# Optimization experiments

Hardware: AMD Instinct MI355X
Metric: run time of the kernel (lower is better)

Reference implementation:

```python
import jax, jax.numpy as jnp
import numpy as np
import math

D = 1024
H = 16
HD = D // H


def setup_inputs() -> dict:
    key = jax.random.key(0)
    ks = jax.random.split(key, 12)
    B, L = 2, 2048
    s = 1.0 / math.sqrt(D)
    inp = {
        "q": jax.random.normal(ks[0], (B, L, D), jnp.float32),
        "k": jax.random.normal(ks[1], (B, L, D), jnp.float32),
        "v": jax.random.normal(ks[2], (B, L, D), jnp.float32),
        "Wq": jax.random.normal(ks[3], (D, D), jnp.float32) * s,
        "bq": jnp.zeros((D,), jnp.float32),
        "Wk": jax.random.normal(ks[4], (D, D), jnp.float32) * s,
        "bk": jnp.zeros((D,), jnp.float32),
        "Wv": jax.random.normal(ks[5], (D, D), jnp.float32) * s,
        "bv": jnp.zeros((D,), jnp.float32),
        "Wo": jax.random.normal(ks[6], (D, D), jnp.float32) * s,
        "bo": jnp.zeros((D,), jnp.float32),
        "P": jax.random.normal(ks[7], (H, H), jnp.float32),  # logit_proj_pre
    }
    return inp


def _split_heads(x, B, L):
    # [B,L,D] -> [B,H,L,HD]
    return x.reshape(B, L, H, HD).transpose(0, 2, 1, 3)


def reference(q, k, v, Wq, bq, Wk, bk, Wv, bv, Wo, bo, P):
    B, L, _ = q.shape
    qh = _split_heads(q @ Wq.T + bq, B, L)
    kh = _split_heads(k @ Wk.T + bk, B, L)
    vh = _split_heads(v @ Wv.T + bv, B, L)
    # raw per-head logits [B,H,L,L]
    logits = jnp.einsum("bhld,bhmd->bhlm", qh, kh) / math.sqrt(HD)
    # talking-heads mixing across heads (pre-softmax)
    logits = jnp.einsum("bhlm,hg->bglm", logits, P)
    attn = jax.nn.softmax(logits, axis=-1)
    out = jnp.einsum("bhlm,bhmd->bhld", attn, vh)  # [B,H,L,HD]
    out = out.transpose(0, 2, 1, 3).reshape(B, L, D)
    return out @ Wo.T + bo
```

## Files before the change

### kernel.cpp

```cpp
#include <hip/hip_runtime.h>

#define D_  1024
#define H_  16
#define HD_ 64
#define L_  2048
#define B_  2
#define M_  (B_*L_)

typedef float f32x4  __attribute__((ext_vector_type(4)));
typedef short bf16x4 __attribute__((ext_vector_type(4)));
typedef short bf16x8 __attribute__((ext_vector_type(8)));

__device__ __forceinline__ float bf2f(short s) {
    return __uint_as_float(((unsigned int)(unsigned short)s) << 16);
}
__device__ __forceinline__ short f2bf(float f) {
    unsigned u = __float_as_uint(f);
    unsigned r = (u + 0x7FFFu + ((u >> 16) & 1u)) >> 16;
    return (short)r;
}

__global__ __launch_bounds__(256) void proj_mfma(
    const float* __restrict__ q, const float* __restrict__ k, const float* __restrict__ v,
    const float* __restrict__ Wq, const float* __restrict__ bq,
    const float* __restrict__ Wk, const float* __restrict__ bk,
    const float* __restrict__ Wv, const float* __restrict__ bv,
    short* __restrict__ qh, short* __restrict__ qlo,
    short* __restrict__ kh, short* __restrict__ vht)
{
    const int z = blockIdx.z;
    const float* X    = (z == 0) ? q  : (z == 1) ? k  : v;
    const float* W    = (z == 0) ? Wq : (z == 1) ? Wk : Wv;
    const float* bias = (z == 0) ? bq : (z == 1) ? bk : bv;

    __shared__ short Ws[128][40];
    __shared__ short Xs[128][40];

    const int tid  = threadIdx.x;
    const int w    = tid >> 6, lane = tid & 63;
    const int l16  = lane & 15, qq = lane >> 4;
    const int m0   = blockIdx.x * 128;
    const int n0   = blockIdx.y * 128;
    const int ar0  = 64 * (w & 1);
    const int br0  = 64 * (w >> 1);

    f32x4 acc[4][4] = {};

    for (int k0 = 0; k0 < D_; k0 += 32) {
        #pragma unroll
        for (int i = 0; i < 4; ++i) {
            int fidx = i * 256 + tid;
            int r = fidx >> 3, c = fidx & 7;
            float4 wv4 = *(const float4*)(W + (size_t)(n0 + r) * D_ + k0 + c * 4);
            float4 xv4 = *(const float4*)(X + (size_t)(m0 + r) * D_ + k0 + c * 4);
            bf16x4 wb = { f2bf(wv4.x), f2bf(wv4.y), f2bf(wv4.z), f2bf(wv4.w) };
            bf16x4 xb = { f2bf(xv4.x), f2bf(xv4.y), f2bf(xv4.z), f2bf(xv4.w) };
            *(bf16x4*)&Ws[r][c * 4] = wb;
            *(bf16x4*)&Xs[r][c * 4] = xb;
        }
        __syncthreads();
        bf16x8 af[4], bfv[4];
        #pragma unroll
        for (int i = 0; i < 4; ++i) {
            const short* Ab = (z < 2) ? &Ws[ar0 + 16 * i + l16][qq * 8]
                                      : &Xs[ar0 + 16 * i + l16][qq * 8];
            const short* Bb = (z < 2) ? &Xs[br0 + 16 * i + l16][qq * 8]
                                      : &Ws[br0 + 16 * i + l16][qq * 8];
            af[i]  = *(const bf16x8*)Ab;
            bfv[i] = *(const bf16x8*)Bb;
        }
        #pragma unroll
        for (int i = 0; i < 4; ++i)
            #pragma unroll
            for (int j = 0; j < 4; ++j)
                acc[i][j] = __builtin_amdgcn_mfma_f32_16x16x32_bf16(af[i], bfv[j], acc[i][j], 0, 0, 0);
        __syncthreads();
    }

    if (z < 2) {
        #pragma unroll
        for (int i = 0; i < 4; ++i) {
            int nb = n0 + ar0 + 16 * i + qq * 4;
            float4 b4 = *(const float4*)(bias + nb);
            int h = nb >> 6, hd = nb & 63;
            #pragma unroll
            for (int j = 0; j < 4; ++j) {
                int m = m0 + br0 + 16 * j + l16;
                int bb = m >> 11, l = m & (L_ - 1);
                size_t o = ((((size_t)bb * H_ + h) * L_) + l) * HD_ + hd;
                f32x4 c = acc[i][j];
                float v0 = c[0] + b4.x, v1 = c[1] + b4.y, v2 = c[2] + b4.z, v3 = c[3] + b4.w;
                bf16x4 hi = { f2bf(v0), f2bf(v1), f2bf(v2), f2bf(v3) };
                if (z == 0) {
                    *(bf16x4*)&qh[o] = hi;
                    bf16x4 lo = { f2bf(v0 - bf2f(hi[0])), f2bf(v1 - bf2f(hi[1])),
                                  f2bf(v2 - bf2f(hi[2])), f2bf(v3 - bf2f(hi[3])) };
                    *(bf16x4*)&qlo[o] = lo;
                } else {
                    *(bf16x4*)&kh[o] = hi;
                }
            }
        }
    } else {
        #pragma unroll
        for (int i = 0; i < 4; ++i) {
            int mb = m0 + ar0 + 16 * i + qq * 4;
            int bb = mb >> 11, lb = mb & (L_ - 1);
            #pragma unroll
            for (int j = 0; j < 4; ++j) {
                int n = n0 + br0 + 16 * j + l16;
                int h = n >> 6, hd = n & 63;
                float bn = bias[n];
                size_t o = (((size_t)bb * H_ + h) * HD_ + hd) * (size_t)L_ + lb;
                f32x4 c = acc[i][j];
                bf16x4 ov = { f2bf(c[0] + bn), f2bf(c[1] + bn), f2bf(c[2] + bn), f2bf(c[3] + bn) };
                *(bf16x4*)&vht[o] = ov;
            }
        }
    }
}

__global__ __launch_bounds__(512, 2) void attn_mfma(
    const short* __restrict__ qh, const short* __restrict__ qlo,
    const short* __restrict__ kh, const short* __restrict__ vht,
    const float* __restrict__ P, short* __restrict__ attn_out)
{
    __shared__ __align__(16) float Sraw[16 * 16 * 20];
    __shared__ __align__(16) short Vslab[8][2 * 64 * 24];
    __shared__ float PmS[256];

    const int tid  = threadIdx.x;
    const int n    = blockIdx.x;
    const int b    = (n >> 2) & 1;
    const int l0   = ((n >> 3) * 4 + (n & 3)) * 16;
    const int w    = tid >> 6, lane = tid & 63;
    const int l16  = lane & 15, qq = lane >> 4;
    const size_t hb = (size_t)b * H_;

    bf16x8 qf[2][2][2];
    #pragma unroll
    for (int hh = 0; hh < 2; ++hh)
        #pragma unroll
        for (int kc = 0; kc < 2; ++kc) {
            size_t off = ((hb + 2 * w + hh) * L_ + l0 + l16) * HD_ + kc * 32 + qq * 8;
            qf[hh][kc][0] = *(const bf16x8*)(qh  + off);
            qf[hh][kc][1] = *(const bf16x8*)(qlo + off);
        }
    bf16x8 kcur[2][2], knxt[2][2], vcur[4], vnxt[4];
    #pragma unroll
    for (int hh = 0; hh < 2; ++hh)
        #pragma unroll
        for (int kc = 0; kc < 2; ++kc)
            kcur[hh][kc] = *(const bf16x8*)(kh + ((hb + 2 * w + hh) * L_ + l16) * HD_ + kc * 32 + qq * 8);
    int vgi_[4], vd_[4];
    const int vc = lane & 1;
    #pragma unroll
    for (int i = 0; i < 4; ++i) {
        int vrow = i * 32 + (lane >> 1);
        vgi_[i] = vrow >> 6;
        vd_[i]  = vrow & 63;
    }
    #pragma unroll
    for (int i = 0; i < 4; ++i)
        vcur[i] = *(const bf16x8*)(vht + ((hb + 2 * w + vgi_[i]) * HD_ + vd_[i]) * (size_t)L_ + vc * 8);

    if (tid < 256) PmS[tid] = P[tid] * 0.125f;
    __syncthreads();

    float pw0[16], pw1[16];
    #pragma unroll
    for (int h = 0; h < 16; ++h) {
        pw0[h] = PmS[h * 16 + 2 * w];
        pw1[h] = PmS[h * 16 + 2 * w + 1];
    }

    f32x4 acc[2][4];
    #pragma unroll
    for (int dt = 0; dt < 4; ++dt) { acc[0][dt] = (f32x4){0.f,0.f,0.f,0.f}; acc[1][dt] = (f32x4){0.f,0.f,0.f,0.f}; }
    float mrun0 = -1e30f, mrun1 = -1e30f, srun0 = 0.f, srun1 = 0.f;

    int vwoff[4];
    #pragma unroll
    for (int i = 0; i < 4; ++i)
        vwoff[i] = vgi_[i] * (64 * 24) + vd_[i] * 24 + vc * 8;

    for (int it = 0; it < 128; ++it) {
        const int mn = ((it + 1) & 127) * 16;
        #pragma unroll
        for (int i = 0; i < 4; ++i)
            *(bf16x8*)&Vslab[w][vwoff[i]] = vcur[i];
        #pragma unroll
        for (int hh = 0; hh < 2; ++hh) {
            f32x4 s = (f32x4){0.f,0.f,0.f,0.f};
            s = __builtin_amdgcn_mfma_f32_16x16x32_bf16(kcur[hh][0], qf[hh][0][0], s, 0, 0, 0);
            s = __builtin_amdgcn_mfma_f32_16x16x32_bf16(kcur[hh][0], qf[hh][0][1], s, 0, 0, 0);
            s = __builtin_amdgcn_mfma_f32_16x16x32_bf16(kcur[hh][1], qf[hh][1][0], s, 0, 0, 0);
            s = __builtin_amdgcn_mfma_f32_16x16x32_bf16(kcur[hh][1], qf[hh][1][1], s, 0, 0, 0);
            *(f32x4*)&Sraw[((2 * w + hh) * 16 + l16) * 20 + qq * 4] = s;
        }
        __syncthreads();
        #pragma unroll
        for (int hh = 0; hh < 2; ++hh)
            #pragma unroll
            for (int kc = 0; kc < 2; ++kc)
                knxt[hh][kc] = *(const bf16x8*)(kh + ((hb + 2 * w + hh) * L_ + mn + l16) * HD_ + kc * 32 + qq * 8);
        #pragma unroll
        for (int i = 0; i < 4; ++i)
            vnxt[i] = *(const bf16x8*)(vht + ((hb + 2 * w + vgi_[i]) * HD_ + vd_[i]) * (size_t)L_ + mn + vc * 8);
        float sx0[4] = {0.f,0.f,0.f,0.f}, sx1[4] = {0.f,0.f,0.f,0.f};
        #pragma unroll
        for (int h = 0; h < 16; ++h) {
            f32x4 c = *(const f32x4*)&Sraw[(h * 16 + l16) * 20 + qq * 4];
            #pragma unroll
            for (int j = 0; j < 4; ++j) { sx0[j] += pw0[h] * c[j]; sx1[j] += pw1[h] * c[j]; }
        }
        float t0 = fmaxf(fmaxf(sx0[0], sx0[1]), fmaxf(sx0[2], sx0[3]));
        float t1 = fmaxf(fmaxf(sx1[0], sx1[1]), fmaxf(sx1[2], sx1[3]));
        t0 = fmaxf(t0, __shfl_xor(t0, 16)); t0 = fmaxf(t0, __shfl_xor(t0, 32));
        t1 = fmaxf(t1, __shfl_xor(t1, 16)); t1 = fmaxf(t1, __shfl_xor(t1, 32));
        float mnew0 = fmaxf(mrun0, t0), mnew1 = fmaxf(mrun1, t1);
        float corr0 = __expf(mrun0 - mnew0), corr1 = __expf(mrun1 - mnew1);
        float e00 = __expf(sx0[0] - mnew0), e01 = __expf(sx0[1] - mnew0);
        float e02 = __expf(sx0[2] - mnew0), e03 = __expf(sx0[3] - mnew0);
        float e10 = __expf(sx1[0] - mnew1), e11 = __expf(sx1[1] - mnew1);
        float e12 = __expf(sx1[2] - mnew1), e13 = __expf(sx1[3] - mnew1);
        float ps0 = e00 + e01 + e02 + e03, ps1 = e10 + e11 + e12 + e13;
        ps0 += __shfl_xor(ps0, 16); ps0 += __shfl_xor(ps0, 32);
        ps1 += __shfl_xor(ps1, 16); ps1 += __shfl_xor(ps1, 32);
        srun0 = srun0 * corr0 + ps0; srun1 = srun1 * corr1 + ps1;
        mrun0 = mnew0; mrun1 = mnew1;
        bf16x4 pf0 = { f2bf(e00), f2bf(e01), f2bf(e02), f2bf(e03) };
        bf16x4 pf1 = { f2bf(e10), f2bf(e11), f2bf(e12), f2bf(e13) };
        acc[0][0] *= corr0; acc[0][1] *= corr0; acc[0][2] *= corr0; acc[0][3] *= corr0;
        acc[1][0] *= corr1; acc[1][1] *= corr1; acc[1][2] *= corr1; acc[1][3] *= corr1;
        #pragma unroll
        for (int i = 0; i < 2; ++i) {
            bf16x4 pf = i ? pf1 : pf0;
            #pragma unroll
            for (int dt = 0; dt < 4; ++dt) {
                bf16x4 afr = *(const bf16x4*)&Vslab[w][i * (64 * 24) + (dt * 16 + l16) * 24 + qq * 4];
                acc[i][dt] = __builtin_amdgcn_mfma_f32_16x16x16bf16_1k(afr, pf, acc[i][dt], 0, 0, 0);
            }
        }
        __syncthreads();
        #pragma unroll
        for (int hh = 0; hh < 2; ++hh)
            #pragma unroll
            for (int kc = 0; kc < 2; ++kc) kcur[hh][kc] = knxt[hh][kc];
        #pragma unroll
        for (int i = 0; i < 4; ++i) vcur[i] = vnxt[i];
    }

    float inv0 = 1.f / srun0, inv1 = 1.f / srun1;
    #pragma unroll
    for (int i = 0; i < 2; ++i) {
        float inv = i ? inv1 : inv0;
        #pragma unroll
        for (int dt = 0; dt < 4; ++dt) {
            f32x4 a = acc[i][dt];
            bf16x4 ov = { f2bf(a[0] * inv), f2bf(a[1] * inv), f2bf(a[2] * inv), f2bf(a[3] * inv) };
            *(bf16x4*)(attn_out + ((size_t)(b * L_ + l0 + l16)) * D_ + (2 * w + i) * 64 + dt * 16 + qq * 4) = ov;
        }
    }
}

__global__ __launch_bounds__(256) void out_mfma(
    const short* __restrict__ attn, const float* __restrict__ Wo,
    const float* __restrict__ bo, float* __restrict__ out)
{
    __shared__ short Ws[128][40];
    __shared__ short Xs[128][40];

    const int tid = threadIdx.x;
    const int w = tid >> 6, lane = tid & 63;
    const int l16 = lane & 15, qq = lane >> 4;
    const int m0 = blockIdx.x * 128;
    const int n0 = blockIdx.y * 128;
    const int ar0 = 64 * (w & 1);
    const int br0 = 64 * (w >> 1);

    f32x4 acc[4][4] = {};

    for (int k0 = 0; k0 < D_; k0 += 32) {
        #pragma unroll
        for (int i = 0; i < 4; ++i) {
            int fidx = i * 256 + tid;
            int r = fidx >> 3, c = fidx & 7;
            float4 wv4 = *(const float4*)(Wo + (size_t)(n0 + r) * D_ + k0 + c * 4);
            bf16x4 wb = { f2bf(wv4.x), f2bf(wv4.y), f2bf(wv4.z), f2bf(wv4.w) };
            *(bf16x4*)&Ws[r][c * 4] = wb;
        }
        #pragma unroll
        for (int i = 0; i < 2; ++i) {
            int cidx = i * 256 + tid;
            int r = cidx >> 2, c = cidx & 3;
            bf16x8 xv = *(const bf16x8*)(attn + (size_t)(m0 + r) * D_ + k0 + c * 8);
            *(bf16x8*)&Xs[r][c * 8] = xv;
        }
        __syncthreads();
        bf16x8 af[4], bfv[4];
        #pragma unroll
        for (int i = 0; i < 4; ++i) {
            af[i]  = *(const bf16x8*)&Ws[ar0 + 16 * i + l16][qq * 8];
            bfv[i] = *(const bf16x8*)&Xs[br0 + 16 * i + l16][qq * 8];
        }
        #pragma unroll
        for (int i = 0; i < 4; ++i)
            #pragma unroll
            for (int j = 0; j < 4; ++j)
                acc[i][j] = __builtin_amdgcn_mfma_f32_16x16x32_bf16(af[i], bfv[j], acc[i][j], 0, 0, 0);
        __syncthreads();
    }

    #pragma unroll
    for (int i = 0; i < 4; ++i) {
        int nb = n0 + ar0 + 16 * i + qq * 4;
        float4 b4 = *(const float4*)(bo + nb);
        #pragma unroll
        for (int j = 0; j < 4; ++j) {
            int m = m0 + br0 + 16 * j + l16;
            f32x4 c = acc[i][j];
            float4 ov = make_float4(c[0] + b4.x, c[1] + b4.y, c[2] + b4.z, c[3] + b4.w);
            *(float4*)&out[(size_t)m * D_ + nb] = ov;
        }
    }
}

extern "C" void kernel_launch(void* const* d_in, const int* in_sizes, int n_in,
                              void* d_out, int out_size, void* d_ws, size_t ws_size,
                              hipStream_t stream) {
    const float* q  = (const float*)d_in[0];
    const float* k  = (const float*)d_in[1];
    const float* v  = (const float*)d_in[2];
    const float* Wq = (const float*)d_in[3];
    const float* bq = (const float*)d_in[4];
    const float* Wk = (const float*)d_in[5];
    const float* bk = (const float*)d_in[6];
    const float* Wv = (const float*)d_in[7];
    const float* bv = (const float*)d_in[8];
    const float* Wo = (const float*)d_in[9];
    const float* bo = (const float*)d_in[10];
    const float* P  = (const float*)d_in[11];
    float* out = (float*)d_out;

    char* ws = (char*)d_ws;
    short* qh   = (short*)(ws);
    short* qlo  = (short*)(ws + (size_t)8 * 1024 * 1024);
    short* kh   = (short*)(ws + (size_t)16 * 1024 * 1024);
    short* vht  = (short*)(ws + (size_t)24 * 1024 * 1024);
    short* attn = (short*)(ws + (size_t)32 * 1024 * 1024);

    proj_mfma<<<dim3(M_ / 128, D_ / 128, 3), 256, 0, stream>>>(
        q, k, v, Wq, bq, Wk, bk, Wv, bv, qh, qlo, kh, vht);
    attn_mfma<<<dim3(256), 512, 0, stream>>>(qh, qlo, kh, vht, P, attn);
    out_mfma<<<dim3(M_ / 128, D_ / 128), 256, 0, stream>>>(attn, Wo, bo, out);
}
```

Baseline: 436.6 us.

## Double-buffer score tile to drop one barrier per step and pad LDS pitches

Restructures the attention loop so the QK^T MFMAs for the next key tile are computed into a second score buffer at the end of each step. This removes one of the two block-wide barriers per iteration, and the loop is unrolled by two with ping-pong K/V register sets prefetched two tiles ahead. It also changes the LDS pitches of the score and V slabs (20→18 floats, 24→36 shorts) and splits the vector stores and loads into narrower pieces, aiming to reduce bank conflicts. The cost is more LDS, more registers for the extra K/V buffers, and narrower LDS accesses, which could hurt occupancy at 512 threads with 2 blocks per CU.

After: 434.9 us. Within noise of the previous version (-0.4%).

```diff
diff --git a/kernel.cpp b/kernel.cpp
--- a/kernel.cpp
+++ b/kernel.cpp
@@ -10,6 +10,9 @@
 typedef float f32x4  __attribute__((ext_vector_type(4)));
 typedef short bf16x4 __attribute__((ext_vector_type(4)));
 typedef short bf16x8 __attribute__((ext_vector_type(8)));
+
+#define SRAW_PITCH 18
+#define VS_PITCH   36
 
 __device__ __forceinline__ float bf2f(short s) {
     return __uint_as_float(((unsigned int)(unsigned short)s) << 16);
@@ -125,8 +128,9 @@
     const short* __restrict__ kh, const short* __restrict__ vht,
     const float* __restrict__ P, short* __restrict__ attn_out)
 {
-    __shared__ __align__(16) float Sraw[16 * 16 * 20];
-    __shared__ __align__(16) short Vslab[8][2 * 64 * 24];
+    __shared__ __align__(16) float Sraw0[16 * 16 * SRAW_PITCH];
+    __shared__ __align__(16) float Sraw1[16 * 16 * SRAW_PITCH];
+    __shared__ __align__(16) short Vslab[8][2 * 64 * VS_PITCH];
     __shared__ float PmS[256];
 
     const int tid  = threadIdx.x;
@@ -146,12 +150,7 @@
             qf[hh][kc][0] = *(const bf16x8*)(qh  + off);
             qf[hh][kc][1] = *(const bf16x8*)(qlo + off);
         }
-    bf16x8 kcur[2][2], knxt[2][2], vcur[4], vnxt[4];
-    #pragma unroll
-    for (int hh = 0; hh < 2; ++hh)
-        #pragma unroll
-        for (int kc = 0; kc < 2; ++kc)
-            kcur[hh][kc] = *(const bf16x8*)(kh + ((hb + 2 * w + hh) * L_ + l16) * HD_ + kc * 32 + qq * 8);
+
     int vgi_[4], vd_[4];
     const int vc = lane & 1;
     #pragma unroll
@@ -160,11 +159,47 @@
         vgi_[i] = vrow >> 6;
         vd_[i]  = vrow & 63;
     }
+    int vwoff[4];
     #pragma unroll
     for (int i = 0; i < 4; ++i)
-        vcur[i] = *(const bf16x8*)(vht + ((hb + 2 * w + vgi_[i]) * HD_ + vd_[i]) * (size_t)L_ + vc * 8);
+        vwoff[i] = vgi_[i] * (64 * VS_PITCH) + vd_[i] * VS_PITCH + vc * 8;
+
+    bf16x8 kA[2][2], kB[2][2], vA[4], vB[4];
+    #pragma unroll
+    for (int hh = 0; hh < 2; ++hh)
+        #pragma unroll
+        for (int kc = 0; kc < 2; ++kc) {
+            kA[hh][kc] = *(const bf16x8*)(kh + ((hb + 2 * w + hh) * L_ + 0  + l16) * HD_ + kc * 32 + qq * 8);
+            kB[hh][kc] = *(const bf16x8*)(kh + ((hb + 2 * w + hh) * L_ + 16 + l16) * HD_ + kc * 32 + qq * 8);
+        }
+    #pragma unroll
+    for (int i = 0; i < 4; ++i) {
+        vA[i] = *(const bf16x8*)(vht + ((hb + 2 * w + vgi_[i]) * HD_ + vd_[i]) * (size_t)L_ + 0  + vc * 8);
+        vB[i] = *(const bf16x8*)(vht + ((hb + 2 * w + vgi_[i]) * HD_ + vd_[i]) * (size_t)L_ + 16 + vc * 8);
+    }
 
     if (tid < 256) PmS[tid] = P[tid] * 0.125f;
+
+    f32x4 acc[2][4];
+    #pragma unroll
+    for (int dt = 0; dt < 4; ++dt) { acc[0][dt] = (f32x4){0.f,0.f,0.f,0.f}; acc[1][dt] = (f32x4){0.f,0.f,0.f,0.f}; }
+    float mrun0 = -1e30f, mrun1 = -1e30f, srun0 = 0.f, srun1 = 0.f;
+
+    auto qkt = [&](bf16x8 (&kr)[2][2], float* sb) {
+        #pragma unroll
+        for (int hh = 0; hh < 2; ++hh) {
+            f32x4 s = (f32x4){0.f,0.f,0.f,0.f};
+            s = __builtin_amdgcn_mfma_f32_16x16x32_bf16(kr[hh][0], qf[hh][0][0], s, 0, 0, 0);
+            s = __builtin_amdgcn_mfma_f32_16x16x32_bf16(kr[hh][0], qf[hh][0][1], s, 0, 0, 0);
+            s = __builtin_amdgcn_mfma_f32_16x16x32_bf16(kr[hh][1], qf[hh][1][0], s, 0, 0, 0);
+            s = __builtin_amdgcn_mfma_f32_16x16x32_bf16(kr[hh][1], qf[hh][1][1], s, 0, 0, 0);
+            float* sp = sb + ((2 * w + hh) * 16 + l16) * SRAW_PITCH + qq * 4;
+            *(float2*)sp       = make_float2(s[0], s[1]);
+            *(float2*)(sp + 2) = make_float2(s[2], s[3]);
+        }
+    };
+
+    qkt(kA, Sraw0);
     __syncthreads();
 
     float pw0[16], pw1[16];
@@ -174,45 +209,36 @@
         pw1[h] = PmS[h * 16 + 2 * w + 1];
     }
 
-    f32x4 acc[2][4];
-    #pragma unroll
-    for (int dt = 0; dt < 4; ++dt) { acc[0][dt] = (f32x4){0.f,0.f,0.f,0.f}; acc[1][dt] = (f32x4){0.f,0.f,0.f,0.f}; }
-    float mrun0 = -1e30f, mrun1 = -1e30f, srun0 = 0.f, srun1 = 0.f;
-
-    int vwoff[4];
-    #pragma unroll
-    for (int i = 0; i < 4; ++i)
-        vwoff[i] = vgi_[i] * (64 * 24) + vd_[i] * 24 + vc * 8;
-
-    for (int it = 0; it < 128; ++it) {
-        const int mn = ((it + 1) & 127) * 16;
-        #pragma unroll
-        for (int i = 0; i < 4; ++i)
-            *(bf16x8*)&Vslab[w][vwoff[i]] = vcur[i];
-        #pragma unroll
-        for (int hh = 0; hh < 2; ++hh) {
-            f32x4 s = (f32x4){0.f,0.f,0.f,0.f};
-            s = __builtin_amdgcn_mfma_f32_16x16x32_bf16(kcur[hh][0], qf[hh][0][0], s, 0, 0, 0);
-            s = __builtin_amdgcn_mfma_f32_16x16x32_bf16(kcur[hh][0], qf[hh][0][1], s, 0, 0, 0);
-            s = __builtin_amdgcn_mfma_f32_16x16x32_bf16(kcur[hh][1], qf[hh][1][0], s, 0, 0, 0);
-            s = __builtin_amdgcn_mfma_f32_16x16x32_bf16(kcur[hh][1], qf[hh][1][1], s, 0, 0, 0);
-            *(f32x4*)&Sraw[((2 * w + hh) * 16 + l16) * 20 + qq * 4] = s;
-        }
-        __syncthreads();
-        #pragma unroll
-        for (int hh = 0; hh < 2; ++hh)
-            #pragma unroll
-            for (int kc = 0; kc < 2; ++kc)
-                knxt[hh][kc] = *(const bf16x8*)(kh + ((hb + 2 * w + hh) * L_ + mn + l16) * HD_ + kc * 32 + qq * 8);
-        #pragma unroll
-        for (int i = 0; i < 4; ++i)
-            vnxt[i] = *(const bf16x8*)(vht + ((hb + 2 * w + vgi_[i]) * HD_ + vd_[i]) * (size_t)L_ + mn + vc * 8);
+    auto body = [&](float* sb, float* sbo, bf16x8 (&vstage)[4], bf16x8 (&kqk)[2][2],
+                    bf16x8 (&kld)[2][2], bf16x8 (&vld)[4], int tnext) {
+        #pragma unroll
+        for (int i = 0; i < 4; ++i) {
+            bf16x4 wlo = { vstage[i][0], vstage[i][1], vstage[i][2], vstage[i][3] };
+            bf16x4 whi = { vstage[i][4], vstage[i][5], vstage[i][6], vstage[i][7] };
+            *(bf16x4*)&Vslab[w][vwoff[i]]     = wlo;
+            *(bf16x4*)&Vslab[w][vwoff[i] + 4] = whi;
+        }
+        {
+            const int mn = tnext * 16;
+            #pragma unroll
+            for (int hh = 0; hh < 2; ++hh)
+                #pragma unroll
+                for (int kc = 0; kc < 2; ++kc)
+                    kld[hh][kc] = *(const bf16x8*)(kh + ((hb + 2 * w + hh) * L_ + mn + l16) * HD_ + kc * 32 + qq * 8);
+            #pragma unroll
+            for (int i = 0; i < 4; ++i)
+                vld[i] = *(const bf16x8*)(vht + ((hb + 2 * w + vgi_[i]) * HD_ + vd_[i]) * (size_t)L_ + mn + vc * 8);
+        }
         float sx0[4] = {0.f,0.f,0.f,0.f}, sx1[4] = {0.f,0.f,0.f,0.f};
         #pragma unroll
         for (int h = 0; h < 16; ++h) {
-            f32x4 c = *(const f32x4*)&Sraw[(h * 16 + l16) * 20 + qq * 4];
-            #pragma unroll
-            for (int j = 0; j < 4; ++j) { sx0[j] += pw0[h] * c[j]; sx1[j] += pw1[h] * c[j]; }
+            const float* sp = sb + (h * 16 + l16) * SRAW_PITCH + qq * 4;
+            float2 ca = *(const float2*)sp;
+            float2 cb = *(const float2*)(sp + 2);
+            sx0[0] += pw0[h] * ca.x; sx0[1] += pw0[h] * ca.y;
+            sx0[2] += pw0[h] * cb.x; sx0[3] += pw0[h] * cb.y;
+            sx1[0] += pw1[h] * ca.x; sx1[1] += pw1[h] * ca.y;
+            sx1[2] += pw1[h] * cb.x; sx1[3] += pw1[h] * cb.y;
         }
         float t0 = fmaxf(fmaxf(sx0[0], sx0[1]), fmaxf(sx0[2], sx0[3]));
         float t1 = fmaxf(fmaxf(sx1[0], sx1[1]), fmaxf(sx1[2], sx1[3]));
@@ -238,17 +264,18 @@
             bf16x4 pf = i ? pf1 : pf0;
             #pragma unroll
             for (int dt = 0; dt < 4; ++dt) {
-                bf16x4 afr = *(const bf16x4*)&Vslab[w][i * (64 * 24) + (dt * 16 + l16) * 24 + qq * 4];
+                bf16x4 afr = *(const bf16x4*)&Vslab[w][i * (64 * VS_PITCH) + (dt * 16 + l16) * VS_PITCH + qq * 4];
                 acc[i][dt] = __builtin_amdgcn_mfma_f32_16x16x16bf16_1k(afr, pf, acc[i][dt], 0, 0, 0);
             }
         }
-        __syncthreads();
-        #pragma unroll
-        for (int hh = 0; hh < 2; ++hh)
-            #pragma unroll
-            for (int kc = 0; kc < 2; ++kc) kcur[hh][kc] = knxt[hh][kc];
-        #pragma unroll
-        for (int i = 0; i < 4; ++i) vcur[i] = vnxt[i];
+        qkt(kqk, sbo);
+        __syncthreads();
+    };
+
+    for (int itp = 0; itp < 64; ++itp) {
+        const int t0 = 2 * itp;
+        body(Sraw0, Sraw1, vA, kB, kA, vA, (t0 + 2) & 127);
+        body(Sraw1, Sraw0, vB, kA, kB, vB, (t0 + 3) & 127);
     }
 
     float inv0 = 1.f / srun0, inv1 = 1.f / srun1;
```
